# Kernel tuning notes

Hardware: AMD Instinct MI355X
Metric: run time of the kernel (lower is better)

Reference implementation:

```python
import jax, jax.numpy as jnp
import numpy as np

B, T, D_IN, H, D_ENC, P, D_ATT = 64, 20, 512, 512, 2048, 196, 512


def setup_inputs() -> dict:
    key = jax.random.key(0)
    ks = jax.random.split(key, 12)
    s = 0.05  # weight scale to keep gates out of saturation
    return {
        "x": jax.random.normal(ks[0], (B, T, D_IN), jnp.float32),
        "cnn_features": jax.random.normal(ks[1], (B, P, D_ENC), jnp.float32),
        "Wi": jax.random.normal(ks[2], (D_IN + H + D_ENC, H), jnp.float32) * s,
        "bi": jnp.zeros((H,), jnp.float32),
        "Wf": jax.random.normal(ks[3], (D_IN + H + D_ENC, H), jnp.float32) * s,
        "bf": jnp.zeros((H,), jnp.float32),
        "Wc": jax.random.normal(ks[4], (D_IN + H + D_ENC, H), jnp.float32) * s,
        "bc": jnp.zeros((H,), jnp.float32),
        "Wo": jax.random.normal(ks[5], (D_IN + H + D_ENC, H), jnp.float32) * s,
        "bo": jnp.zeros((H,), jnp.float32),
        "Wa_feat": jax.random.normal(ks[6], (D_ENC, D_ATT), jnp.float32) * s,
        "Wa_h": jax.random.normal(ks[7], (H, D_ATT), jnp.float32) * s,
        "ba": jnp.zeros((D_ATT,), jnp.float32),
        "v": jax.random.normal(ks[8], (D_ATT,), jnp.float32) * s,
    }


def reference(x, cnn_features, Wi, bi, Wf, bf, Wc, bc, Wo, bo, Wa_feat, Wa_h, ba, v):
    batch, seq_len, _ = x.shape
    hid = Wi.shape[1]
    # feature projection is h-independent: hoist out of the time loop
    feat_proj = jnp.einsum('bpe,ea->bpa', cnn_features, Wa_feat) + ba  # [B,P,A]

    def step(carry, x_t):
        h, c = carry
        # additive (Bahdanau) attention over pixels
        e = jnp.einsum('bpa,a->bp', jnp.tanh(feat_proj + (h @ Wa_h)[:, None, :]), v)
        alpha = jax.nn.softmax(e, axis=-1)                      # [B,P]
        ctx = jnp.einsum('bp,bpe->be', alpha, cnn_features)     # [B,E]
        comb = jnp.concatenate([x_t, h, ctx], axis=1)           # [B,D_IN+H+E]
        i_t = jax.nn.sigmoid(comb @ Wi + bi)
        f_t = jax.nn.sigmoid(comb @ Wf + bf)
        o_t = jax.nn.sigmoid(comb @ Wo + bo)
        c_tilde = jnp.tanh(comb @ Wc + bc)
        c_new = f_t * c + i_t * c_tilde
        h_new = o_t * jnp.tanh(c_new)
        return (h_new, c_new), h_new

    h0 = jnp.zeros((batch, hid), x.dtype)
    c0 = jnp.zeros((batch, hid), x.dtype)
    (h_T, c_T), ys = jax.lax.scan(step, (h0, c0), jnp.swapaxes(x, 0, 1))
    outputs = jnp.swapaxes(ys, 0, 1)  # [B,T,H]
    return outputs, h_T, c_T
```

## Files before the change

### kernel.cpp

```cpp
#include <hip/hip_runtime.h>

typedef unsigned short u16;
typedef unsigned int u32;
typedef __attribute__((ext_vector_type(8))) short bf16x8;
typedef __attribute__((ext_vector_type(4))) float f32x4;

#define NB 64
#define NT 20
#define NH 512
#define NP 196
#define NE 2048
#define NA 512

__device__ __forceinline__ u16 f2bf(float f) {
  u32 b = __float_as_uint(f);
  return (u16)((b + 0x7FFFu + ((b >> 16) & 1u)) >> 16);
}
__device__ __forceinline__ float bf2f(u16 u) { return __uint_as_float(((u32)u) << 16); }
__device__ __forceinline__ float tanh_fast(float x) {
  float xc = fminf(fmaxf(x, -15.f), 15.f);
  float e2 = __builtin_amdgcn_exp2f(xc * 2.885390082f);
  return (e2 - 1.f) * __builtin_amdgcn_rcpf(e2 + 1.f);
}
__device__ __forceinline__ float sigmoid_fast(float x) {
  return __builtin_amdgcn_rcpf(1.f + __builtin_amdgcn_exp2f(x * -1.44269504f));
}

__device__ __forceinline__ void gload_lds16(const u16* g, u16* l) {
  __builtin_amdgcn_global_load_lds((const __attribute__((address_space(1))) void*)g,
                                   (__attribute__((address_space(3))) void*)l, 16, 0, 0);
}

template <int N>
__device__ __forceinline__ void vwait() {
  if constexpr (N >= 0)
    asm volatile("s_waitcnt vmcnt(%0)" ::"i"(N) : "memory");
  else
    asm volatile("" ::: "memory");
}

__global__ __launch_bounds__(256) void conv_bf16(const float4* __restrict__ src,
                                                 u16* __restrict__ dst, int n4) {
  int i = blockIdx.x * 256 + threadIdx.x;
  int stride = gridDim.x * 256;
  for (; i < n4; i += stride) {
    float4 v = src[i];
    u32 lo = (u32)f2bf(v.x) | ((u32)f2bf(v.y) << 16);
    u32 hi = (u32)f2bf(v.z) | ((u32)f2bf(v.w) << 16);
    *(uint2*)(dst + (size_t)i * 4) = make_uint2(lo, hi);
  }
}

__global__ __launch_bounds__(128) void conv_x(const float* __restrict__ x,
                                              u16* __restrict__ xbT) {
  int b = blockIdx.x, t = blockIdx.y, tid = threadIdx.x;
  float4 v = *(const float4*)(x + ((size_t)b * NT + t) * 512 + tid * 4);
  u32 lo = (u32)f2bf(v.x) | ((u32)f2bf(v.y) << 16);
  u32 hi = (u32)f2bf(v.z) | ((u32)f2bf(v.w) << 16);
  *(uint2*)(xbT + ((size_t)t * NB + b) * 512 + tid * 4) = make_uint2(lo, hi);
}

__global__ __launch_bounds__(256) void transpose_w(const float* __restrict__ W0,
                                                   const float* __restrict__ W1,
                                                   const float* __restrict__ W2,
                                                   const float* __restrict__ W3,
                                                   u16* __restrict__ dst, int row_off, int K) {
  const float* src = blockIdx.z == 0 ? W0 : blockIdx.z == 1 ? W1 : blockIdx.z == 2 ? W2 : W3;
  __shared__ float tile[32][33];
  int k0 = blockIdx.x * 32, n0 = blockIdx.y * 32;
  int tx = threadIdx.x & 31, ty = threadIdx.x >> 5;
#pragma unroll
  for (int i = 0; i < 4; ++i)
    tile[ty + i * 8][tx] = src[(size_t)(row_off + k0 + ty + i * 8) * 512 + n0 + tx];
  __syncthreads();
#pragma unroll
  for (int i = 0; i < 4; ++i) {
    int n = n0 + ty + i * 8, k = k0 + tx;
    dst[((size_t)blockIdx.z * 512 + n) * K + k] = f2bf(tile[tx][ty + i * 8]);
  }
}

__global__ __launch_bounds__(256) void gemm_bf16(const u16* __restrict__ A,
                                                 const u16* __restrict__ BT,
                                                 float* __restrict__ C, int M, int N, int K) {
  __shared__ u16 lA[128 * 64];
  __shared__ u16 lB[128 * 64];
  const int tid = threadIdx.x;
  const int lane = tid & 63;
  const int wid = tid >> 6;
  const int m0 = blockIdx.x * 128, n0 = blockIdx.y * 128;
  const int wm = (wid >> 1) * 64, wn = (wid & 1) * 64;
  f32x4 acc[4][4] = {};

  const int cbase = wid * 256;
  int srcr[4], srcc[4];
#pragma unroll
  for (int it = 0; it < 4; ++it) {
    int c = cbase + it * 64 + lane;
    srcr[it] = c >> 3;
    srcc[it] = ((c & 7) ^ ((c >> 3) & 7)) * 8;
  }

  for (int k0 = 0; k0 < K; k0 += 64) {
    __syncthreads();
#pragma unroll
    for (int it = 0; it < 4; ++it) {
      gload_lds16(A + (size_t)(m0 + srcr[it]) * K + k0 + srcc[it],
                  lA + (size_t)(cbase + it * 64) * 8);
      gload_lds16(BT + (size_t)(n0 + srcr[it]) * K + k0 + srcc[it],
                  lB + (size_t)(cbase + it * 64) * 8);
    }
    __syncthreads();
#pragma unroll
    for (int kk = 0; kk < 2; ++kk) {
      int kchunk = kk * 4 + (lane >> 4);
      bf16x8 af[4], bg[4];
#pragma unroll
      for (int i = 0; i < 4; ++i) {
        int row = wm + i * 16 + (lane & 15);
        af[i] = *(const bf16x8*)(lA + row * 64 + ((kchunk ^ (row & 7)) * 8));
        int rowb = wn + i * 16 + (lane & 15);
        bg[i] = *(const bf16x8*)(lB + rowb * 64 + ((kchunk ^ (rowb & 7)) * 8));
      }
#pragma unroll
      for (int i = 0; i < 4; ++i)
#pragma unroll
        for (int j = 0; j < 4; ++j)
          acc[i][j] = __builtin_amdgcn_mfma_f32_16x16x32_bf16(af[i], bg[j], acc[i][j], 0, 0, 0);
    }
  }
#pragma unroll
  for (int i = 0; i < 4; ++i) {
    int m = m0 + wm + i * 16 + ((lane >> 4) * 4);
#pragma unroll
    for (int j = 0; j < 4; ++j) {
      int n = n0 + wn + j * 16 + (lane & 15);
#pragma unroll
      for (int r = 0; r < 4; ++r) C[(size_t)(m + r) * N + n] = acc[i][j][r];
    }
  }
}

#define PHASE(MH, NH, LA, LB, CUR, DOSTAGE, MATB, HH, K1, WN)                             \
  do {                                                                                    \
    const u16* pA_ = lds + (CUR) * 32768;                                                 \
    const u16* pB_ = pA_ + 16384;                                                         \
    if (LA) {                                                                             \
      _Pragma("unroll") for (int kh_ = 0; kh_ < 2; ++kh_) {                               \
        const int kc_ = kh_ * 4 + (lane >> 4);                                            \
        _Pragma("unroll") for (int i_ = 0; i_ < 4; ++i_) {                                \
          const int rw_ = (MH) * 128 + wmB + i_ * 16 + l15;                               \
          af[kh_][i_] = *(const bf16x8*)(pA_ + rw_ * 64 + ((kc_ ^ (rw_ & 7)) * 8));       \
        }                                                                                 \
      }                                                                                   \
    }                                                                                     \
    if (LB) {                                                                             \
      _Pragma("unroll") for (int kh_ = 0; kh_ < 2; ++kh_) {                               \
        const int kc_ = kh_ * 4 + (lane >> 4);                                            \
        _Pragma("unroll") for (int j_ = 0; j_ < 2; ++j_) {                                \
          const int rw_ = (NH) * 128 + wnB + j_ * 16 + l15;                               \
          bg[kh_][j_] = *(const bf16x8*)(pB_ + rw_ * 64 + ((kc_ ^ (rw_ & 7)) * 8));       \
        }                                                                                 \
      }                                                                                   \
    }                                                                                     \
    if (DOSTAGE) {                                                                        \
      const u16* gsrc_ = (MATB) ? BT : A;                                                 \
      const int r0_ = (MATB) ? n0 : m0;                                                   \
      u16* ldst_ = lds + (1 - (CUR)) * 32768 + (MATB) * 16384;                            \
      _Pragma("unroll") for (int s_ = 0; s_ < 2; ++s_)                                    \
          gload_lds16(gsrc_ + (size_t)(r0_ + srcR[HH][s_]) * K + (K1) + srcC[HH][s_],     \
                      ldst_ + ldsOff[HH][s_]);                                            \
    }                                                                                     \
    vwait<WN>();                                                                          \
    __builtin_amdgcn_s_barrier();                                                         \
    __builtin_amdgcn_s_setprio(1);                                                        \
    _Pragma("unroll") for (int kh_ = 0; kh_ < 2; ++kh_)                                   \
      _Pragma("unroll") for (int i_ = 0; i_ < 4; ++i_)                                    \
        _Pragma("unroll") for (int j_ = 0; j_ < 2; ++j_)                                  \
          acc[(MH) * 4 + i_][(NH) * 2 + j_] = __builtin_amdgcn_mfma_f32_16x16x32_bf16(    \
              af[kh_][i_], bg[kh_][j_], acc[(MH) * 4 + i_][(NH) * 2 + j_], 0, 0, 0);      \
    __builtin_amdgcn_s_setprio(0);                                                        \
    __builtin_amdgcn_s_barrier();                                                         \
  } while (0)

__global__ __launch_bounds__(512, 2) void gemm256(const u16* __restrict__ A,
                                                  const u16* __restrict__ BT,
                                                  const float* __restrict__ bias,
                                                  u16* __restrict__ fpb, u16* __restrict__ cnW,
                                                  int K, int grid_n) {
  __shared__ u16 lds[65536];
  const int tid = threadIdx.x;
  const int lane = tid & 63;
  const int wid = tid >> 6;
  const int l15 = lane & 15;
  const int nblk = gridDim.x;
  const int q = nblk >> 3, rr = nblk & 7;
  const int xcd = blockIdx.x & 7, jj = blockIdx.x >> 3;
  const int swz = (xcd < rr ? xcd * (q + 1) : rr * (q + 1) + (xcd - rr) * q) + jj;
  const int mt = swz / grid_n, nt = swz - mt * grid_n;
  const int m0 = mt * 256, n0 = nt * 256;
  const int wmB = (wid >> 2) * 64;
  const int wnB = (wid & 3) * 32;
  f32x4 acc[8][4] = {};
  bf16x8 af[2][4], bg[2][2];

  int srcR[2][2], srcC[2][2], ldsOff[2][2];
#pragma unroll
  for (int h = 0; h < 2; ++h)
#pragma unroll
    for (int s = 0; s < 2; ++s) {
      int c = h * 1024 + s * 512 + wid * 64 + lane;
      srcR[h][s] = c >> 3;
      srcC[h][s] = ((c & 7) ^ ((c >> 3) & 7)) * 8;
      ldsOff[h][s] = (h * 1024 + s * 512 + wid * 64) * 8;
    }

#pragma unroll
  for (int s = 0; s < 2; ++s)
    gload_lds16(A + (size_t)(m0 + srcR[0][s]) * K + srcC[0][s], lds + ldsOff[0][s]);
#pragma unroll
  for (int s = 0; s < 2; ++s)
    gload_lds16(BT + (size_t)(n0 + srcR[0][s]) * K + srcC[0][s], lds + 16384 + ldsOff[0][s]);
#pragma unroll
  for (int s = 0; s < 2; ++s)
    gload_lds16(A + (size_t)(m0 + srcR[1][s]) * K + srcC[1][s], lds + ldsOff[1][s]);
#pragma unroll
  for (int s = 0; s < 2; ++s)
    gload_lds16(BT + (size_t)(n0 + srcR[1][s]) * K + srcC[1][s], lds + 16384 + ldsOff[1][s]);
  vwait<4>();
  __builtin_amdgcn_s_barrier();

  const int KT = K >> 6;
  for (int kt = 0; kt < KT - 1; ++kt) {
    const int cur = kt & 1;
    const int k1 = (kt + 1) << 6;
    PHASE(0, 0, 1, 1, cur, 1, 0, 0, k1, 4);
    PHASE(1, 0, 1, 0, cur, 1, 1, 0, k1, 4);
    PHASE(1, 1, 0, 1, cur, 1, 0, 1, k1, -1);
    PHASE(0, 1, 1, 0, cur, 1, 1, 1, k1, 4);
  }
  {
    const int cur = (KT - 1) & 1;
    PHASE(0, 0, 1, 1, cur, 0, 0, 0, 0, 2);
    PHASE(1, 0, 1, 0, cur, 0, 0, 0, 0, 0);
    PHASE(1, 1, 0, 1, cur, 0, 0, 0, 0, -1);
    PHASE(0, 1, 1, 0, cur, 0, 0, 0, 0, -1);
  }

#pragma unroll
  for (int i = 0; i < 8; ++i) {
    int m = m0 + (i >> 2) * 128 + wmB + (i & 3) * 16 + ((lane >> 4) * 4);
#pragma unroll
    for (int j = 0; j < 4; ++j) {
      int n = n0 + (j >> 1) * 128 + wnB + (j & 1) * 16 + l15;
      float bv = (n < 512) ? bias[n] : 0.f;
#pragma unroll
      for (int r = 0; r < 4; ++r) {
        float val = acc[i][j][r] + bv;
        u32 me = (u32)(m + r);
        if (n < 512) {
          fpb[(size_t)me * 512 + n] = f2bf(val);
        } else {
          u32 bdx = me / 196u;
          u32 p = me - bdx * 196u;
          u32 g = (u32)(n - 512) >> 9;
          u32 n9 = (u32)(n - 512) & 511u;
          cnW[(((size_t)bdx * 4 + g) * 196 + p) * 512 + n9] = f2bf(val);
        }
      }
    }
  }
}

__global__ __launch_bounds__(256) void hproj(const u16* __restrict__ hprev,
                                             const u16* __restrict__ wcT,
                                             float* __restrict__ hp) {
  const int ntile = blockIdx.x;
  const int tid = threadIdx.x, lane = tid & 63, kh = tid >> 6;
  const int l15 = lane & 15;
  const u16* Bp = wcT + (size_t)(ntile * 16 + l15) * 512 + kh * 128 + ((lane >> 4) * 8);
  const u16* Ap = hprev + (size_t)l15 * 512 + kh * 128 + ((lane >> 4) * 8);
  f32x4 acc[4] = {};
#pragma unroll
  for (int ks = 0; ks < 4; ++ks) {
    bf16x8 bb = *(const bf16x8*)(Bp + ks * 32);
#pragma unroll
    for (int mf = 0; mf < 4; ++mf) {
      bf16x8 a = *(const bf16x8*)(Ap + (size_t)mf * 16 * 512 + ks * 32);
      acc[mf] = __builtin_amdgcn_mfma_f32_16x16x32_bf16(a, bb, acc[mf], 0, 0, 0);
    }
  }
  __shared__ float pre[4][64][16];
  const int rrow = (lane >> 4) * 4;
#pragma unroll
  for (int mf = 0; mf < 4; ++mf)
#pragma unroll
    for (int r = 0; r < 4; ++r) pre[kh][mf * 16 + rrow + r][l15] = acc[mf][r];
  __syncthreads();
  const int m = tid >> 2, n = (tid & 3) * 4;
  float4 s;
  float* sp = (float*)&s;
#pragma unroll
  for (int j = 0; j < 4; ++j)
    sp[j] = pre[0][m][n + j] + pre[1][m][n + j] + pre[2][m][n + j] + pre[3][m][n + j];
  *(float4*)(hp + (size_t)m * 2560 + ntile * 16 + n) = s;
}

__global__ __launch_bounds__(1024) void attn_gates(
    const u16* __restrict__ fpb, const float* __restrict__ hp, const float* __restrict__ v,
    const u16* __restrict__ cw, const float* __restrict__ xw, const float* __restrict__ bi,
    const float* __restrict__ bfg, const float* __restrict__ bc, const float* __restrict__ bo,
    float* __restrict__ cbuf, float* __restrict__ out, u16* __restrict__ hnext, int t) {
  const int b = blockIdx.x & 63;
  const int quarter = blockIdx.x >> 6;
  const int tid = threadIdx.x;
  const int lane = tid & 63, wid = tid >> 6;
  __shared__ float smem_a[1024];
  __shared__ float sm[16];
  __shared__ float alp[200];
  __shared__ float red[8192];

  float* hwa = smem_a;
  float* vv = smem_a + 512;
  if (tid < 512) {
    hwa[tid] = (t > 0) ? hp[(size_t)b * 2560 + 2048 + tid] : 0.f;
    vv[tid] = v[tid];
  }
  if (tid >= 196 && tid < 256) red[tid] = -3e38f;
  __syncthreads();

  float hw[8], vr[8];
#pragma unroll
  for (int j = 0; j < 8; ++j) {
    hw[j] = hwa[lane * 8 + j];
    vr[j] = vv[lane * 8 + j];
  }
  for (int p = wid; p < NP; p += 16) {
    const u16* fp = fpb + ((size_t)b * NP + p) * 512 + lane * 8;
    uint4 raw = *(const uint4*)fp;
    u32 w[4] = {raw.x, raw.y, raw.z, raw.w};
    float part = 0.f;
#pragma unroll
    for (int j = 0; j < 8; ++j) {
      u16 u = (u16)(w[j >> 1] >> ((j & 1) * 16));
      part += tanh_fast(bf2f(u) + hw[j]) * vr[j];
    }
#pragma unroll
    for (int off = 32; off > 0; off >>= 1) part += __shfl_xor(part, off);
    if (lane == 0) red[p] = part;
  }
  __syncthreads();

  float ev = 0.f, w = 0.f;
  if (tid < 256) {
    ev = red[tid];
    float m_ = ev;
#pragma unroll
    for (int off = 32; off > 0; off >>= 1) m_ = fmaxf(m_, __shfl_xor(m_, off));
    if (lane == 0) sm[wid] = m_;
  }
  __syncthreads();
  if (tid < 256) {
    float mx = fmaxf(fmaxf(sm[0], sm[1]), fmaxf(sm[2], sm[3]));
    w = (tid < NP) ? __builtin_amdgcn_exp2f((ev - mx) * 1.44269504f) : 0.f;
    float s_ = w;
#pragma unroll
    for (int off = 32; off > 0; off >>= 1) s_ += __shfl_xor(s_, off);
    if (lane == 0) sm[8 + wid] = s_;
  }
  __syncthreads();
  if (tid < NP) {
    float tot = (sm[8] + sm[9]) + (sm[10] + sm[11]);
    alp[tid] = w * __builtin_amdgcn_rcpf(tot);
  }
  __syncthreads();

  {
    const int g = tid >> 8, pg = (tid >> 4) & 15, colc = tid & 15;
    const u16* base = cw + ((size_t)(b * 4 + g) * 196) * 512 + quarter * 128 + colc * 8;
    float acc[8] = {};
    for (int i = 0; i < 13; ++i) {
      int p = pg + i * 16;
      if (p < NP) {
        float al = alp[p];
        uint4 raw = *(const uint4*)(base + (size_t)p * 512);
        u32 wds[4] = {raw.x, raw.y, raw.z, raw.w};
#pragma unroll
        for (int j = 0; j < 8; ++j) acc[j] += al * bf2f((u16)(wds[j >> 1] >> ((j & 1) * 16)));
      }
    }
#pragma unroll
    for (int j = 0; j < 8; ++j) red[((g * 16 + pg) * 16 + colc) * 8 + j] = acc[j];
  }
  __syncthreads();

  float* pre4 = smem_a;
  if (tid < 512) {
    const int g = tid >> 7, nn = tid & 127;
    float s = 0.f;
#pragma unroll
    for (int pg = 0; pg < 16; ++pg) s += red[((g * 16 + pg) * 16 + (nn >> 3)) * 8 + (nn & 7)];
    pre4[g * 128 + nn] = s;
  }
  __syncthreads();

  if (tid < 128) {
    const int ng = quarter * 128 + tid;
    const size_t xwo = ((size_t)t * NB + b) * 2048;
    const size_t hpb = (size_t)b * 2560;
    float hwh0 = 0.f, hwh1 = 0.f, hwh2 = 0.f, hwh3 = 0.f;
    if (t > 0) {
      hwh0 = hp[hpb + ng];
      hwh1 = hp[hpb + 512 + ng];
      hwh2 = hp[hpb + 1024 + ng];
      hwh3 = hp[hpb + 1536 + ng];
    }
    float ip = pre4[0 * 128 + tid] + xw[xwo + ng] + hwh0 + bi[ng];
    float fp = pre4[1 * 128 + tid] + xw[xwo + 512 + ng] + hwh1 + bfg[ng];
    float cp = pre4[2 * 128 + tid] + xw[xwo + 1024 + ng] + hwh2 + bc[ng];
    float op = pre4[3 * 128 + tid] + xw[xwo + 1536 + ng] + hwh3 + bo[ng];
    float it = sigmoid_fast(ip), ft = sigmoid_fast(fp), ot = sigmoid_fast(op);
    float ctl = tanh_fast(cp);
    float cold = (t > 0) ? cbuf[(size_t)b * 512 + ng] : 0.f;
    float cn = ft * cold + it * ctl;
    float hn = ot * tanh_fast(cn);
    cbuf[(size_t)b * 512 + ng] = cn;
    hnext[(size_t)b * 512 + ng] = f2bf(hn);
    out[((size_t)b * NT + t) * 512 + ng] = hn;
    if (t == NT - 1) {
      out[(size_t)NB * NT * 512 + (size_t)b * 512 + ng] = hn;
      out[(size_t)NB * NT * 512 + (size_t)NB * 512 + (size_t)b * 512 + ng] = cn;
    }
  }
}

extern "C" void kernel_launch(void* const* d_in, const int* in_sizes, int n_in, void* d_out,
                              int out_size, void* d_ws, size_t ws_size, hipStream_t stream) {
  const float* x = (const float*)d_in[0];
  const float* cnn = (const float*)d_in[1];
  const float* Wi = (const float*)d_in[2];
  const float* bi = (const float*)d_in[3];
  const float* Wf = (const float*)d_in[4];
  const float* bfv = (const float*)d_in[5];
  const float* Wc = (const float*)d_in[6];
  const float* bc = (const float*)d_in[7];
  const float* Wo = (const float*)d_in[8];
  const float* bo = (const float*)d_in[9];
  const float* Waf = (const float*)d_in[10];
  const float* Wah = (const float*)d_in[11];
  const float* ba = (const float*)d_in[12];
  const float* v = (const float*)d_in[13];
  float* out = (float*)d_out;

  char* base = (char*)d_ws;
  size_t off = 0;
  auto alloc = [&](size_t bytes) {
    char* r = base + off;
    off += (bytes + 255) & ~(size_t)255;
    return r;
  };
  u16* cnnb = (u16*)alloc((size_t)NB * NP * NE * 2);
  u16* fpb = (u16*)alloc((size_t)NB * NP * NA * 2);
  u16* cnW = (u16*)alloc((size_t)NB * 4 * NP * 512 * 2);
  u16* wbig = (u16*)alloc((size_t)2560 * 2048 * 2);
  u16* wcombT = (u16*)alloc((size_t)2560 * 512 * 2);
  u16* wxt = (u16*)alloc((size_t)4 * 512 * 512 * 2);
  u16* xbT = (u16*)alloc((size_t)NT * NB * 512 * 2);
  float* xw = (float*)alloc((size_t)NT * NB * 2048 * 4);
  u16* hbuf = (u16*)alloc((size_t)2 * NB * 512 * 2);
  float* cbuf = (float*)alloc((size_t)NB * 512 * 4);
  float* hp = (float*)alloc((size_t)NB * 2560 * 4);

  (void)ws_size;
  (void)in_sizes;
  (void)n_in;
  (void)out_size;

  conv_bf16<<<2048, 256, 0, stream>>>((const float4*)cnn, cnnb, (NB * NP * NE) / 4);
  conv_x<<<dim3(NB, NT), 128, 0, stream>>>(x, xbT);
  {
    dim3 g1(512 / 32, 16, 4);
    transpose_w<<<g1, 256, 0, stream>>>(Wi, Wf, Wc, Wo, wxt, 0, 512);
    dim3 g2(2048 / 32, 16, 1);
    transpose_w<<<g2, 256, 0, stream>>>(Waf, Waf, Waf, Waf, wbig, 0, 2048);
    dim3 g3(2048 / 32, 16, 4);
    transpose_w<<<g3, 256, 0, stream>>>(Wi, Wf, Wc, Wo, wbig + (size_t)512 * 2048, 1024, 2048);
    dim3 g4(512 / 32, 16, 4);
    transpose_w<<<g4, 256, 0, stream>>>(Wi, Wf, Wc, Wo, wcombT, 512, 512);
    dim3 g5(512 / 32, 16, 1);
    transpose_w<<<g5, 256, 0, stream>>>(Wah, Wah, Wah, Wah, wcombT + (size_t)2048 * 512, 0, 512);
  }

  gemm256<<<49 * 10, 512, 0, stream>>>(cnnb, wbig, ba, fpb, cnW, 2048, 10);

  {
    dim3 g(1280 / 128, 2048 / 128);
    gemm_bf16<<<g, 256, 0, stream>>>(xbT, wxt, xw, 1280, 2048, 512);
  }

  for (int t = 0; t < NT; ++t) {
    const u16* hprev = hbuf + (size_t)(t & 1) * NB * 512;
    u16* hnext = hbuf + (size_t)((t + 1) & 1) * NB * 512;
    if (t > 0) hproj<<<160, 256, 0, stream>>>(hprev, wcombT, hp);
    attn_gates<<<256, 1024, 0, stream>>>(fpb, hp, v, cnW, xw, bi, bfv, bc, bo, cbuf, out, hnext,
                                         t);
  }
}
```

Baseline: 675.4 us.

## Restructure gemm256 warp tiling to 128x64 per wave with B fragments reused across phases

Changes each wave's sub-tile in the 256x256 GEMM from two separate 64x32 quadrants to a contiguous 128x64 block. B fragments for the whole k-step are read once from LDS in the first phase and reused across four phases, each of which loads only two A fragments. Global-to-LDS staging of the next k-tile is concentrated into the first two phases with a single wait at the end of the iteration. The aim is to cut LDS read traffic per MFMA and simplify the pipeline, at the cost of holding more B fragments in registers and changing the overlap between loads and compute.

```diff
diff --git a/kernel.cpp b/kernel.cpp
--- a/kernel.cpp
+++ b/kernel.cpp
@@ -141,46 +141,48 @@
   }
 }
 
-#define PHASE(MH, NH, LA, LB, CUR, DOSTAGE, MATB, HH, K1, WN)                             \
-  do {                                                                                    \
-    const u16* pA_ = lds + (CUR) * 32768;                                                 \
-    const u16* pB_ = pA_ + 16384;                                                         \
-    if (LA) {                                                                             \
-      _Pragma("unroll") for (int kh_ = 0; kh_ < 2; ++kh_) {                               \
-        const int kc_ = kh_ * 4 + (lane >> 4);                                            \
-        _Pragma("unroll") for (int i_ = 0; i_ < 4; ++i_) {                                \
-          const int rw_ = (MH) * 128 + wmB + i_ * 16 + l15;                               \
-          af[kh_][i_] = *(const bf16x8*)(pA_ + rw_ * 64 + ((kc_ ^ (rw_ & 7)) * 8));       \
-        }                                                                                 \
-      }                                                                                   \
-    }                                                                                     \
-    if (LB) {                                                                             \
-      _Pragma("unroll") for (int kh_ = 0; kh_ < 2; ++kh_) {                               \
-        const int kc_ = kh_ * 4 + (lane >> 4);                                            \
-        _Pragma("unroll") for (int j_ = 0; j_ < 2; ++j_) {                                \
-          const int rw_ = (NH) * 128 + wnB + j_ * 16 + l15;                               \
-          bg[kh_][j_] = *(const bf16x8*)(pB_ + rw_ * 64 + ((kc_ ^ (rw_ & 7)) * 8));       \
-        }                                                                                 \
-      }                                                                                   \
-    }                                                                                     \
-    if (DOSTAGE) {                                                                        \
-      const u16* gsrc_ = (MATB) ? BT : A;                                                 \
-      const int r0_ = (MATB) ? n0 : m0;                                                   \
-      u16* ldst_ = lds + (1 - (CUR)) * 32768 + (MATB) * 16384;                            \
-      _Pragma("unroll") for (int s_ = 0; s_ < 2; ++s_)                                    \
-          gload_lds16(gsrc_ + (size_t)(r0_ + srcR[HH][s_]) * K + (K1) + srcC[HH][s_],     \
-                      ldst_ + ldsOff[HH][s_]);                                            \
-    }                                                                                     \
-    vwait<WN>();                                                                          \
-    __builtin_amdgcn_s_barrier();                                                         \
-    __builtin_amdgcn_s_setprio(1);                                                        \
-    _Pragma("unroll") for (int kh_ = 0; kh_ < 2; ++kh_)                                   \
-      _Pragma("unroll") for (int i_ = 0; i_ < 4; ++i_)                                    \
-        _Pragma("unroll") for (int j_ = 0; j_ < 2; ++j_)                                  \
-          acc[(MH) * 4 + i_][(NH) * 2 + j_] = __builtin_amdgcn_mfma_f32_16x16x32_bf16(    \
-              af[kh_][i_], bg[kh_][j_], acc[(MH) * 4 + i_][(NH) * 2 + j_], 0, 0, 0);      \
-    __builtin_amdgcn_s_setprio(0);                                                        \
-    __builtin_amdgcn_s_barrier();                                                         \
+#define STG(SS, CUR, K1)                                                                    \
+  do {                                                                                      \
+    _Pragma("unroll") for (int q_ = 0; q_ < 2; ++q_) {                                      \
+      const u16* g_ = ((SS) < 2)                                                            \
+                          ? (A + (size_t)(m0 + sR[SS][q_]) * K + (K1) + sC[SS][q_])         \
+                          : (BT + (size_t)(n0 + sR[SS][q_]) * K + (K1) + sC[SS][q_]);       \
+      gload_lds16(g_, lds + ((CUR) ^ 1) * 32768 + sL[SS][q_]);                              \
+    }                                                                                       \
+  } while (0)
+
+#define PH(MF0, READB, CUR, DOSTAGE, SB, K1, WN)                                            \
+  do {                                                                                      \
+    const u16* pA_ = lds + (CUR) * 32768;                                                   \
+    const u16* pB_ = pA_ + 16384;                                                           \
+    bf16x8 af_[2][2];                                                                       \
+    _Pragma("unroll") for (int kh_ = 0; kh_ < 2; ++kh_) {                                   \
+      const int kc_ = kh_ * 4 + (lane >> 4);                                                \
+      _Pragma("unroll") for (int ii_ = 0; ii_ < 2; ++ii_) {                                 \
+        const int rA_ = wmH * 128 + ((MF0) + ii_) * 16 + l15;                               \
+        af_[kh_][ii_] = *(const bf16x8*)(pA_ + rA_ * 64 + ((kc_ ^ (rA_ & 7)) * 8));         \
+      }                                                                                     \
+      if (READB) {                                                                          \
+        _Pragma("unroll") for (int j_ = 0; j_ < 4; ++j_) {                                  \
+          const int rB_ = wnq * 64 + j_ * 16 + l15;                                         \
+          bg[kh_][j_] = *(const bf16x8*)(pB_ + rB_ * 64 + ((kc_ ^ (rB_ & 7)) * 8));         \
+        }                                                                                   \
+      }                                                                                     \
+    }                                                                                       \
+    if (DOSTAGE) {                                                                          \
+      STG(SB, CUR, K1);                                                                     \
+      STG((SB) + 1, CUR, K1);                                                               \
+    }                                                                                       \
+    vwait<WN>();                                                                            \
+    __builtin_amdgcn_s_barrier();                                                           \
+    __builtin_amdgcn_s_setprio(1);                                                          \
+    _Pragma("unroll") for (int kh_ = 0; kh_ < 2; ++kh_)                                     \
+      _Pragma("unroll") for (int ii_ = 0; ii_ < 2; ++ii_)                                   \
+        _Pragma("unroll") for (int j_ = 0; j_ < 4; ++j_)                                    \
+          acc[(MF0) + ii_][j_] = __builtin_amdgcn_mfma_f32_16x16x32_bf16(                   \
+              af_[kh_][ii_], bg[kh_][j_], acc[(MF0) + ii_][j_], 0, 0, 0);                   \
+    __builtin_amdgcn_s_setprio(0);                                                          \
+    __builtin_amdgcn_s_barrier();                                                           \
   } while (0)
 
 __global__ __launch_bounds__(512, 2) void gemm256(const u16* __restrict__ A,
@@ -199,60 +201,54 @@
   const int swz = (xcd < rr ? xcd * (q + 1) : rr * (q + 1) + (xcd - rr) * q) + jj;
   const int mt = swz / grid_n, nt = swz - mt * grid_n;
   const int m0 = mt * 256, n0 = nt * 256;
-  const int wmB = (wid >> 2) * 64;
-  const int wnB = (wid & 3) * 32;
+  const int wmH = wid >> 2;
+  const int wnq = wid & 3;
   f32x4 acc[8][4] = {};
-  bf16x8 af[2][4], bg[2][2];
-
-  int srcR[2][2], srcC[2][2], ldsOff[2][2];
-#pragma unroll
-  for (int h = 0; h < 2; ++h)
-#pragma unroll
-    for (int s = 0; s < 2; ++s) {
-      int c = h * 1024 + s * 512 + wid * 64 + lane;
-      srcR[h][s] = c >> 3;
-      srcC[h][s] = ((c & 7) ^ ((c >> 3) & 7)) * 8;
-      ldsOff[h][s] = (h * 1024 + s * 512 + wid * 64) * 8;
-    }
-
-#pragma unroll
-  for (int s = 0; s < 2; ++s)
-    gload_lds16(A + (size_t)(m0 + srcR[0][s]) * K + srcC[0][s], lds + ldsOff[0][s]);
-#pragma unroll
-  for (int s = 0; s < 2; ++s)
-    gload_lds16(BT + (size_t)(n0 + srcR[0][s]) * K + srcC[0][s], lds + 16384 + ldsOff[0][s]);
-#pragma unroll
-  for (int s = 0; s < 2; ++s)
-    gload_lds16(A + (size_t)(m0 + srcR[1][s]) * K + srcC[1][s], lds + ldsOff[1][s]);
-#pragma unroll
-  for (int s = 0; s < 2; ++s)
-    gload_lds16(BT + (size_t)(n0 + srcR[1][s]) * K + srcC[1][s], lds + 16384 + ldsOff[1][s]);
-  vwait<4>();
+  bf16x8 bg[2][4];
+
+  int sR[4][2], sC[4][2], sL[4][2];
+#pragma unroll
+  for (int s = 0; s < 4; ++s)
+#pragma unroll
+    for (int qq = 0; qq < 2; ++qq) {
+      int reg = (s < 2) ? s : s - 2;
+      int ra = reg * 1024 + qq * 512 + wid * 64;
+      int idx = ra + lane;
+      sR[s][qq] = idx >> 3;
+      sC[s][qq] = ((idx & 7) ^ ((idx >> 3) & 7)) * 8;
+      sL[s][qq] = ((s < 2) ? 0 : 16384) + ra * 8;
+    }
+
+  STG(0, 1, 0);
+  STG(1, 1, 0);
+  STG(2, 1, 0);
+  STG(3, 1, 0);
+  vwait<0>();
   __builtin_amdgcn_s_barrier();
 
   const int KT = K >> 6;
   for (int kt = 0; kt < KT - 1; ++kt) {
     const int cur = kt & 1;
     const int k1 = (kt + 1) << 6;
-    PHASE(0, 0, 1, 1, cur, 1, 0, 0, k1, 4);
-    PHASE(1, 0, 1, 0, cur, 1, 1, 0, k1, 4);
-    PHASE(1, 1, 0, 1, cur, 1, 0, 1, k1, -1);
-    PHASE(0, 1, 1, 0, cur, 1, 1, 1, k1, 4);
+    PH(0, 1, cur, 1, 0, k1, -1);
+    PH(2, 0, cur, 1, 2, k1, -1);
+    PH(4, 0, cur, 0, 0, 0, -1);
+    PH(6, 0, cur, 0, 0, 0, 0);
   }
   {
     const int cur = (KT - 1) & 1;
-    PHASE(0, 0, 1, 1, cur, 0, 0, 0, 0, 2);
-    PHASE(1, 0, 1, 0, cur, 0, 0, 0, 0, 0);
-    PHASE(1, 1, 0, 1, cur, 0, 0, 0, 0, -1);
-    PHASE(0, 1, 1, 0, cur, 0, 0, 0, 0, -1);
+    PH(0, 1, cur, 0, 0, 0, -1);
+    PH(2, 0, cur, 0, 0, 0, -1);
+    PH(4, 0, cur, 0, 0, 0, -1);
+    PH(6, 0, cur, 0, 0, 0, -1);
   }
 
 #pragma unroll
   for (int i = 0; i < 8; ++i) {
-    int m = m0 + (i >> 2) * 128 + wmB + (i & 3) * 16 + ((lane >> 4) * 4);
+    int m = m0 + wmH * 128 + i * 16 + ((lane >> 4) * 4);
 #pragma unroll
     for (int j = 0; j < 4; ++j) {
-      int n = n0 + (j >> 1) * 128 + wnB + (j & 1) * 16 + l15;
+      int n = n0 + wnq * 64 + j * 16 + l15;
       float bv = (n < 512) ? bias[n] : 0.f;
 #pragma unroll
       for (int r = 0; r < 4; ++r) {
```

Measured after the change: 672.5 us. Within noise of the previous version (-0.4%).
